# Optimization experiments

Measured on AMD Instinct MI355X. Metric: run time of the kernel, lower is better.

## Reference

```python
import jax, jax.numpy as jnp
import numpy as np
from jax import lax

DIM = 192
HEADS = 4
HIDDEN = int(DIM * 2.66)  # 510


def _conv1x1(x, w, b):
    # x: [B,C,H,W], w: [O,C], b: [O]
    return jnp.einsum('bchw,oc->bohw', x, w) + b[None, :, None, None]


def _dwconv3x3(x, w, b):
    # x: [B,C,H,W], w: [C,1,3,3], b: [C]
    c = x.shape[1]
    y = lax.conv_general_dilated(x, w, window_strides=(1, 1), padding='SAME',
                                 feature_group_count=c,
                                 dimension_numbers=('NCHW', 'OIHW', 'NCHW'))
    return y + b[None, :, None, None]


def _layernorm_c(x, w, b):
    # LayerNorm over channel dim (torch LayerNorm(dim) applied to b,(hw),c)
    mu = jnp.mean(x, axis=1, keepdims=True)
    var = jnp.mean((x - mu) ** 2, axis=1, keepdims=True)
    xn = (x - mu) / jnp.sqrt(var + 1e-5)
    return xn * w[None, :, None, None] + b[None, :, None, None]


def _l2norm(x):
    # F.normalize(dim=-1), eps=1e-12
    n = jnp.sqrt(jnp.sum(x * x, axis=-1, keepdims=True))
    return x / jnp.maximum(n, 1e-12)


def setup_inputs() -> dict:
    key = jax.random.key(0)
    ks = jax.random.split(key, 16)
    s = 0.02
    d, h2 = DIM, HIDDEN * 2
    return {
        'x': jax.random.normal(ks[0], (4, DIM, 128, 128), jnp.float32),
        'ln1_w': jnp.ones((d,), jnp.float32),
        'ln1_b': jnp.zeros((d,), jnp.float32),
        'qkv_w': jax.random.normal(ks[1], (3 * d, d), jnp.float32) * s,
        'qkv_b': jnp.zeros((3 * d,), jnp.float32),
        'qkv_dw_w': jax.random.normal(ks[2], (3 * d, 1, 3, 3), jnp.float32) * s,
        'qkv_dw_b': jnp.zeros((3 * d,), jnp.float32),
        'temperature': jnp.ones((HEADS, 1, 1), jnp.float32),
        'proj_w': jax.random.normal(ks[3], (d, d), jnp.float32) * s,
        'proj_b': jnp.zeros((d,), jnp.float32),
        'ln2_w': jnp.ones((d,), jnp.float32),
        'ln2_b': jnp.zeros((d,), jnp.float32),
        'pin_w': jax.random.normal(ks[4], (h2, d), jnp.float32) * s,
        'pin_b': jnp.zeros((h2,), jnp.float32),
        'dw_w': jax.random.normal(ks[5], (h2, 1, 3, 3), jnp.float32) * s,
        'dw_b': jnp.zeros((h2,), jnp.float32),
        'pout_w': jax.random.normal(ks[6], (d, HIDDEN), jnp.float32) * s,
        'pout_b': jnp.zeros((d,), jnp.float32),
    }


def _attention(x, qkv_w, qkv_b, qkv_dw_w, qkv_dw_b, temperature, proj_w, proj_b):
    b, c, h, w = x.shape
    qkv = _dwconv3x3(_conv1x1(x, qkv_w, qkv_b), qkv_dw_w, qkv_dw_b)
    q, k, v = jnp.split(qkv, 3, axis=1)
    ch = c // HEADS

    def heads(t):  # b (head c) h w -> b head c (h w)
        return t.reshape(b, HEADS, ch, h * w)

    q, k, v = heads(q), heads(k), heads(v)
    q = _l2norm(q)
    k = _l2norm(k)
    attn = jnp.einsum('bhcn,bhdn->bhcd', q, k) * temperature[None]  # [b,H,ch,ch]
    attn = jax.nn.softmax(attn, axis=-1)
    out = jnp.einsum('bhcd,bhdn->bhcn', attn, v)
    out = out.reshape(b, c, h, w)
    return _conv1x1(out, proj_w, proj_b)


def _ffn(x, pin_w, pin_b, dw_w, dw_b, pout_w, pout_b):
    y = _conv1x1(x, pin_w, pin_b)
    y = _dwconv3x3(y, dw_w, dw_b)
    x1, x2 = jnp.split(y, 2, axis=1)
    y = jax.nn.gelu(x1, approximate=False) * x2
    return _conv1x1(y, pout_w, pout_b)


def reference(x, ln1_w, ln1_b, qkv_w, qkv_b, qkv_dw_w, qkv_dw_b, temperature,
              proj_w, proj_b, ln2_w, ln2_b, pin_w, pin_b, dw_w, dw_b,
              pout_w, pout_b):
    x = x + _attention(_layernorm_c(x, ln1_w, ln1_b), qkv_w, qkv_b,
                       qkv_dw_w, qkv_dw_b, temperature, proj_w, proj_b)
    x = x + _ffn(_layernorm_c(x, ln2_w, ln2_b), pin_w, pin_b, dw_w, dw_b,
                 pout_w, pout_b)
    return x
```

## Files before the change

### kernel.cpp

```cpp
#include <hip/hip_runtime.h>
#include <math.h>

typedef long long i64;
typedef unsigned short u16;
typedef unsigned int u32;

#define HW 16384
#define DIM 192
#define NHEADS 4
#define CH 48
#define OQKV 576
#define HID 510
#define H2 1020
#define NB 4
#define NSPLIT 64
#define QKSTR 264

typedef __attribute__((ext_vector_type(8))) short short8v;
typedef __attribute__((ext_vector_type(4))) float float4v;

__device__ __forceinline__ u32 pk(float a, float b) {
  u32 r;
  asm("v_cvt_pk_bf16_f32 %0, %1, %2" : "=v"(r) : "v"(a), "v"(b));
  return r;
}
__device__ __forceinline__ u16 f2bf(float f) {
  union { float f; u32 u; } v; v.f = f;
  u32 r = v.u + 0x7FFF + ((v.u >> 16) & 1);
  return (u16)(r >> 16);
}
__device__ __forceinline__ float bflo(u32 w) {
  union { u32 u; float f; } v; v.u = w << 16; return v.f;
}
__device__ __forceinline__ float bfhi(u32 w) {
  union { u32 u; float f; } v; v.u = w & 0xFFFF0000u; return v.f;
}
__device__ __forceinline__ float bf1(u16 h) {
  union { u32 u; float f; } v; v.u = ((u32)h) << 16; return v.f;
}
__device__ __forceinline__ float gelu_s(float x) {
  return x / (1.f + __expf(-1.702f * x));
}

#define GLL16(gp, lp) __builtin_amdgcn_global_load_lds( \
    (const __attribute__((address_space(1))) u32*)(gp), \
    (__attribute__((address_space(3))) u32*)(lp), 16, 0, 0)

__global__ __launch_bounds__(256) void ln_kernel(const float* __restrict__ x,
    const float* __restrict__ w, const float* __restrict__ b, u16* __restrict__ yT) {
  __shared__ float st[32][193];
  __shared__ float red[2][8][32];
  __shared__ float murs[2][32];
  const float* xb = x + (i64)blockIdx.y * DIM * HW;
  u16* yb = yT + (i64)blockIdx.y * (i64)HW * DIM;
  int tid = threadIdx.x;
  int g = tid >> 5, p = tid & 31;
  int pix0 = blockIdx.x * 32;
  float s = 0.f, ss = 0.f;
  #pragma unroll
  for (int i = 0; i < 24; ++i) {
    float t = xb[(i64)(g * 24 + i) * HW + pix0 + p];
    st[p][g * 24 + i] = t; s += t; ss += t * t;
  }
  red[0][g][p] = s; red[1][g][p] = ss;
  __syncthreads();
  if (tid < 32) {
    float S = 0.f, SS = 0.f;
    #pragma unroll
    for (int gg = 0; gg < 8; ++gg) { S += red[0][gg][tid]; SS += red[1][gg][tid]; }
    float mu = S * (1.f / DIM);
    float var = SS * (1.f / DIM) - mu * mu;
    murs[0][tid] = mu;
    murs[1][tid] = rsqrtf(var + 1e-5f);
  }
  __syncthreads();
  int px = tid >> 3, c0 = (tid & 7) * 24;
  float mu = murs[0][px], rs = murs[1][px];
  u32 ob[12];
  #pragma unroll
  for (int i = 0; i < 24; i += 2) {
    float va = (st[px][c0 + i + 0] - mu) * rs * w[c0 + i + 0] + b[c0 + i + 0];
    float vb = (st[px][c0 + i + 1] - mu) * rs * w[c0 + i + 1] + b[c0 + i + 1];
    ob[i >> 1] = pk(va, vb);
  }
  u16* yp = yb + (i64)(pix0 + px) * DIM + c0;
  #pragma unroll
  for (int j = 0; j < 3; ++j) *(uint4*)(yp + j * 8) = *(const uint4*)&ob[j * 4];
}

__global__ __launch_bounds__(256) void wconv_all(const float* __restrict__ qkv_w,
    const float* __restrict__ proj_w, const float* __restrict__ pin_w,
    const float* __restrict__ pout_w, u16* __restrict__ Wq, u16* __restrict__ Wpj,
    u16* __restrict__ Wpi, u16* __restrict__ Wpo) {
  int idx = blockIdx.x * 256 + threadIdx.x;
  const float* src; u16* dst; int O, C, Kpad;
  if (idx < 122880)      { src = qkv_w;  dst = Wq;  O = OQKV; C = 192; Kpad = 192; }
  else if (idx < 172032) { idx -= 122880; src = proj_w; dst = Wpj; O = 192;  C = 192; Kpad = 192; }
  else if (idx < 368640) { idx -= 172032; src = pin_w;  dst = Wpi; O = H2;   C = 192; Kpad = 192; }
  else if (idx < 499712) { idx -= 368640; src = pout_w; dst = Wpo; O = 192;  C = HID; Kpad = 512; }
  else return;
  int r = idx / Kpad, c = idx - r * Kpad;
  dst[idx] = f2bf((r < O && c < C) ? src[(i64)r * C + c] : 0.f);
}

__global__ __launch_bounds__(256) void gemm_bf16(const u16* __restrict__ A,
    const float* __restrict__ bias, const u16* __restrict__ B,
    const float* __restrict__ Res, float* __restrict__ Out,
    u16* __restrict__ OutB, int O, int K, i64 sB, i64 sOut, i64 sRes) {
  __shared__ __align__(16) u16 lds[2 * 128 * 64];
  int zb = blockIdx.z;
  B += (i64)zb * sB;
  if (Res) Res += (i64)zb * sRes;
  if (OutB) OutB += (i64)zb * sOut; else Out += (i64)zb * sOut;
  int tid = threadIdx.x;
  int lane = tid & 63, wave = tid >> 6;
  int wm = (wave >> 1) * 64, wn = (wave & 1) * 64;
  int obase = blockIdx.y * 128, nbase = blockIdx.x * 128;
  float4v acc[4][4];
  #pragma unroll
  for (int m = 0; m < 4; ++m)
    #pragma unroll
    for (int n = 0; n < 4; ++n) acc[m][n] = (float4v){0.f, 0.f, 0.f, 0.f};

  const u16* Abase = A + (i64)obase * K;
  const u16* Bbase = B + (i64)nbase * K;
  char* ldsA = (char*)&lds[0];
  char* ldsB = (char*)&lds[8192];
  int srow = wave * 8 + (lane >> 3);
  int sj = lane & 7;

  for (int k0 = 0; k0 < K; k0 += 64) {
    #pragma unroll
    for (int iss = 0; iss < 4; ++iss) {
      int r = iss * 32 + srow;
      int kb = sj ^ (r & 7);
      GLL16(Abase + (i64)r * K + k0 + kb * 8, ldsA + iss * 4096 + wave * 1024);
      GLL16(Bbase + (i64)r * K + k0 + kb * 8, ldsB + iss * 4096 + wave * 1024);
    }
    __syncthreads();
    #pragma unroll
    for (int kk = 0; kk < 2; ++kk) {
      short8v af[4], bfr[4];
      #pragma unroll
      for (int m = 0; m < 4; ++m) {
        int r = wm + m * 16 + (lane & 15);
        int kb = kk * 4 + (lane >> 4);
        af[m] = *(const short8v*)(ldsA + r * 128 + ((kb ^ (r & 7)) << 4));
      }
      #pragma unroll
      for (int n = 0; n < 4; ++n) {
        int r = wn + n * 16 + (lane & 15);
        int kb = kk * 4 + (lane >> 4);
        bfr[n] = *(const short8v*)(ldsB + r * 128 + ((kb ^ (r & 7)) << 4));
      }
      #pragma unroll
      for (int m = 0; m < 4; ++m)
        #pragma unroll
        for (int n = 0; n < 4; ++n)
          acc[m][n] = __builtin_amdgcn_mfma_f32_16x16x32_bf16(af[m], bfr[n], acc[m][n], 0, 0, 0);
    }
    __syncthreads();
  }

  int rowq = lane >> 4, coln = lane & 15;
  if (OutB) {
    #pragma unroll
    for (int m = 0; m < 4; ++m) {
      #pragma unroll
      for (int reg = 0; reg < 4; ++reg) {
        int o = wm + m * 16 + rowq * 4 + reg;
        int oo = obase + o;
        float bv = (oo < O) ? bias[oo] : 0.f;
        #pragma unroll
        for (int n = 0; n < 4; n += 2) {
          u32 w2 = pk(acc[m][n][reg] + bv, acc[m][n + 1][reg] + bv);
          lds[o * 128 + wn + n * 16 + coln] = (u16)w2;
          lds[o * 128 + wn + (n + 1) * 16 + coln] = (u16)(w2 >> 16);
        }
      }
    }
    __syncthreads();
    const u32* st32 = (const u32*)lds;
    #pragma unroll
    for (int k = 0; k < 32; ++k) {
      int idx = k * 256 + tid;
      int o = idx >> 6, cd = idx & 63;
      if (obase + o < O)
        ((u32*)(OutB + (i64)(obase + o) * HW + nbase))[cd] = st32[o * 64 + cd];
    }
  } else {
    #pragma unroll
    for (int m = 0; m < 4; ++m) {
      #pragma unroll
      for (int reg = 0; reg < 4; ++reg) {
        int o = obase + wm + m * 16 + rowq * 4 + reg;
        if (o >= O) continue;
        float bv = bias[o];
        #pragma unroll
        for (int n = 0; n < 4; ++n) {
          int nn = nbase + wn + n * 16 + coln;
          float v = acc[m][n][reg] + bv;
          if (Res) v += Res[(i64)o * HW + nn];
          Out[(i64)o * HW + nn] = v;
        }
      }
    }
  }
}

__global__ __launch_bounds__(64) void gemm_skinny(const u16* __restrict__ A,
    const float* __restrict__ bias, const u16* __restrict__ B,
    const float* __restrict__ Res, float* __restrict__ Out,
    int K, i64 sB, i64 sOut, i64 sRes) {
  int zb = blockIdx.y;
  B   += (i64)zb * sB;
  Res += (i64)zb * sRes;
  Out += (i64)zb * sOut;
  int lane = threadIdx.x;
  int r = lane & 15, kq = lane >> 4;
  int nbase = blockIdx.x * 32;
  float4v acc[12][2];
  #pragma unroll
  for (int mi = 0; mi < 12; ++mi) {
    acc[mi][0] = (float4v){0.f, 0.f, 0.f, 0.f};
    acc[mi][1] = (float4v){0.f, 0.f, 0.f, 0.f};
  }
  const u16* Ap = A + (i64)r * K + kq * 8;
  const u16* Bp0 = B + (i64)(nbase + r) * K + kq * 8;
  const u16* Bp1 = Bp0 + (i64)16 * K;
  for (int ks = 0; ks < K; ks += 32) {
    short8v b0 = *(const short8v*)(Bp0 + ks);
    short8v b1 = *(const short8v*)(Bp1 + ks);
    #pragma unroll
    for (int mi = 0; mi < 12; ++mi) {
      short8v a = *(const short8v*)(Ap + (i64)mi * 16 * K + ks);
      acc[mi][0] = __builtin_amdgcn_mfma_f32_16x16x32_bf16(a, b0, acc[mi][0], 0, 0, 0);
      acc[mi][1] = __builtin_amdgcn_mfma_f32_16x16x32_bf16(a, b1, acc[mi][1], 0, 0, 0);
    }
  }
  #pragma unroll
  for (int mi = 0; mi < 12; ++mi) {
    #pragma unroll
    for (int reg = 0; reg < 4; ++reg) {
      int o = mi * 16 + kq * 4 + reg;
      float bv = bias[o];
      #pragma unroll
      for (int ni = 0; ni < 2; ++ni) {
        int n = nbase + ni * 16 + r;
        Out[(i64)o * HW + n] = acc[mi][ni][reg] + bv + Res[(i64)o * HW + n];
      }
    }
  }
}

__global__ __launch_bounds__(256) void dwconv_bf16(const u16* __restrict__ in,
    const float* __restrict__ w9, const float* __restrict__ bs,
    u16* __restrict__ out) {
  in  += (i64)blockIdx.z * OQKV * HW;
  out += (i64)blockIdx.z * OQKV * HW;
  int q = threadIdx.x & 31;
  int grp = threadIdx.x >> 5;
  int y0 = blockIdx.y * 2;
  int c0 = blockIdx.x * 64 + grp * 8;
  int xb = q * 4;
  #pragma unroll
  for (int i = 0; i < 8; ++i) {
    int c = c0 + i;
    const float* wp = w9 + c * 9;
    float bv = bs[c];
    const u16* chan = in + (i64)c * HW;
    float f[4][6];
    #pragma unroll
    for (int r4 = 0; r4 < 4; ++r4) {
      int yy = y0 - 1 + r4;
      if (yy < 0 || yy >= 128) {
        #pragma unroll
        for (int e = 0; e < 6; ++e) f[r4][e] = 0.f;
      } else {
        uint4 raw = *(const uint4*)(chan + yy * 128 + xb - 2);
        f[r4][0] = (q == 0) ? 0.f : bfhi(raw.x);
        f[r4][1] = bflo(raw.y); f[r4][2] = bfhi(raw.y);
        f[r4][3] = bflo(raw.z); f[r4][4] = bfhi(raw.z);
        f[r4][5] = (q == 31) ? 0.f : bflo(raw.w);
      }
    }
    #pragma unroll
    for (int rr = 0; rr < 2; ++rr) {
      float a0 = bv, a1 = bv, a2 = bv, a3 = bv;
      #pragma unroll
      for (int dy = 0; dy < 3; ++dy) {
        float wa = wp[dy * 3 + 0], wb = wp[dy * 3 + 1], wc = wp[dy * 3 + 2];
        const float* fr = f[rr + dy];
        a0 += wa * fr[0] + wb * fr[1] + wc * fr[2];
        a1 += wa * fr[1] + wb * fr[2] + wc * fr[3];
        a2 += wa * fr[2] + wb * fr[3] + wc * fr[4];
        a3 += wa * fr[3] + wb * fr[4] + wc * fr[5];
      }
      uint2 o2;
      o2.x = pk(a0, a1);
      o2.y = pk(a2, a3);
      *(uint2*)(out + (i64)c * HW + (y0 + rr) * 128 + xb) = o2;
    }
  }
}

__global__ __launch_bounds__(256) void l2inv_bf16(const u16* __restrict__ qkv,
    float* __restrict__ inv) {
  int ch = blockIdx.x;
  const u16* p = qkv + (i64)blockIdx.y * OQKV * HW + (i64)ch * HW;
  float s = 0.f;
  for (int i = threadIdx.x * 8; i < HW; i += 256 * 8) {
    uint4 raw = *(const uint4*)(p + i);
    float v0 = bflo(raw.x), v1 = bfhi(raw.x);
    float v2 = bflo(raw.y), v3 = bfhi(raw.y);
    float v4 = bflo(raw.z), v5 = bfhi(raw.z);
    float v6 = bflo(raw.w), v7 = bfhi(raw.w);
    s += v0 * v0 + v1 * v1 + v2 * v2 + v3 * v3 + v4 * v4 + v5 * v5 + v6 * v6 + v7 * v7;
  }
  #pragma unroll
  for (int m = 32; m; m >>= 1) s += __shfl_xor(s, m);
  __shared__ float wsum[4];
  int lane = threadIdx.x & 63, wid = threadIdx.x >> 6;
  if (lane == 0) wsum[wid] = s;
  __syncthreads();
  if (threadIdx.x == 0) {
    float t = wsum[0] + wsum[1] + wsum[2] + wsum[3];
    inv[(i64)blockIdx.y * 384 + ch] = 1.f / fmaxf(sqrtf(t), 1e-12f);
  }
}

__global__ __launch_bounds__(256) void attn_qk_mfma(const u16* __restrict__ qkv,
    float* __restrict__ part) {
  qkv  += (i64)blockIdx.z * OQKV * HW;
  part += (i64)blockIdx.z * 589824;
  __shared__ __align__(16) u16 qs[48][QKSTR];
  __shared__ __align__(16) u16 ks[48][QKSTR];
  int h = blockIdx.x, spb = blockIdx.y;
  int n0 = spb * 1024;
  const u16* qb = qkv + (i64)(h * CH) * HW;
  const u16* kb = qkv + (i64)(DIM + h * CH) * HW;
  int tid = threadIdx.x;
  int lane = tid & 63, wave = tid >> 6;
  float4v acc[3][3];
  #pragma unroll
  for (int i = 0; i < 3; ++i)
    #pragma unroll
    for (int j = 0; j < 3; ++j) acc[i][j] = (float4v){0.f, 0.f, 0.f, 0.f};

  for (int it = 0; it < 4; ++it) {
    int base = n0 + it * 256;
    for (int l = tid; l < 1536; l += 256) {
      int r = l >> 5, j = (l & 31) * 8;
      *(uint4*)&qs[r][j] = *(const uint4*)(qb + (i64)r * HW + base + j);
      *(uint4*)&ks[r][j] = *(const uint4*)(kb + (i64)r * HW + base + j);
    }
    __syncthreads();
    int kbase = wave * 64;
    #pragma unroll
    for (int ksi = 0; ksi < 2; ++ksi) {
      int kofs = kbase + ksi * 32 + (lane >> 4) * 8;
      short8v aq[3], bk[3];
      #pragma unroll
      for (int t = 0; t < 3; ++t) {
        aq[t] = *(const short8v*)&qs[t * 16 + (lane & 15)][kofs];
        bk[t] = *(const short8v*)&ks[t * 16 + (lane & 15)][kofs];
      }
      #pragma unroll
      for (int ci = 0; ci < 3; ++ci)
        #pragma unroll
        for (int di = 0; di < 3; ++di)
          acc[ci][di] = __builtin_amdgcn_mfma_f32_16x16x32_bf16(aq[ci], bk[di], acc[ci][di], 0, 0, 0);
    }
    __syncthreads();
  }
  int rowq = lane >> 4, coln = lane & 15;
  float* pp = part + ((i64)(h * NSPLIT) + spb * 4 + wave) * 2304;
  #pragma unroll
  for (int ci = 0; ci < 3; ++ci)
    #pragma unroll
    for (int reg = 0; reg < 4; ++reg) {
      int c = ci * 16 + rowq * 4 + reg;
      #pragma unroll
      for (int di = 0; di < 3; ++di)
        pp[c * 48 + di * 16 + coln] = acc[ci][di][reg];
    }
}

__global__ __launch_bounds__(64) void attn_sm3(const float* __restrict__ part,
    const float* __restrict__ inv, const float* __restrict__ temp,
    float* __restrict__ attn) {
  part += (i64)blockIdx.z * 589824;
  attn += (i64)blockIdx.z * 9216;
  const float* invb = inv + (i64)blockIdx.z * 384;
  int h = blockIdx.x, c = blockIdx.y;
  int d = threadIdx.x;
  float logit = -1e30f;
  if (d < CH) {
    float s = 0.f;
    for (int sp = 0; sp < NSPLIT; ++sp)
      s += part[((i64)(h * NSPLIT) + sp) * 2304 + c * 48 + d];
    logit = s * invb[h * CH + c] * invb[192 + h * CH + d] * temp[h];
  }
  float m = logit;
  #pragma unroll
  for (int mask = 32; mask; mask >>= 1) m = fmaxf(m, __shfl_xor(m, mask));
  float e = (d < CH) ? expf(logit - m) : 0.f;
  float ssum = e;
  #pragma unroll
  for (int mask = 32; mask; mask >>= 1) ssum += __shfl_xor(ssum, mask);
  if (d < CH) attn[(i64)h * 2304 + c * 48 + d] = e / ssum;
}

__global__ __launch_bounds__(256) void attn_v_kernel(const u16* __restrict__ qkv,
    const float* __restrict__ attnm, u16* __restrict__ outT) {
  qkv   += (i64)blockIdx.z * OQKV * HW;
  attnm += (i64)blockIdx.z * 9216;
  outT  += (i64)blockIdx.z * (i64)HW * DIM;
  __shared__ float as[CH * CH];
  __shared__ u16 st[256 * 52];
  int h = blockIdx.x, tile = blockIdx.y;
  int tid = threadIdx.x;
  for (int l = tid; l < CH * CH; l += 256) as[l] = attnm[(i64)h * 2304 + l];
  __syncthreads();
  int n = tile * 256 + tid;
  const u16* vb = qkv + (i64)(2 * DIM + h * CH) * HW + n;
  float vreg[CH];
  #pragma unroll
  for (int d = 0; d < CH; ++d) vreg[d] = bf1(vb[(i64)d * HW]);
  u32* strow = (u32*)st + tid * 26;
  #pragma unroll 2
  for (int c = 0; c < CH; c += 4) {
    float a0 = 0.f, a1 = 0.f, a2 = 0.f, a3 = 0.f;
    const float* r0 = &as[(c + 0) * CH];
    const float* r1 = &as[(c + 1) * CH];
    const float* r2 = &as[(c + 2) * CH];
    const float* r3 = &as[(c + 3) * CH];
    #pragma unroll
    for (int d = 0; d < CH; ++d) {
      float vv = vreg[d];
      a0 += r0[d] * vv; a1 += r1[d] * vv; a2 += r2[d] * vv; a3 += r3[d] * vv;
    }
    strow[(c >> 1) + 0] = pk(a0, a1);
    strow[(c >> 1) + 1] = pk(a2, a3);
  }
  __syncthreads();
  const uint2* sv = (const uint2*)st;
  u16* ob = outT + (i64)(tile * 256) * DIM + h * CH;
  #pragma unroll
  for (int k = 0; k < 12; ++k) {
    int idx = k * 256 + tid;
    int px = idx / 12, pc = idx - px * 12;
    *(uint2*)(ob + (i64)px * DIM + pc * 4) = sv[px * 13 + pc];
  }
}

__global__ __launch_bounds__(256) void dwgate_bf16(const u16* __restrict__ h1,
    const float* __restrict__ w9, const float* __restrict__ bs,
    u16* __restrict__ og) {
  h1 += (i64)blockIdx.z * H2 * HW;
  og += (i64)blockIdx.z * (i64)HW * 512;
  __shared__ u32 st[128 * 17];
  int q = threadIdx.x & 31;
  int grp = threadIdx.x >> 5;
  int y = blockIdx.y;
  int c0 = blockIdx.x * 32 + grp * 4;
  int xb = q * 4;
  float prev[4];
  #pragma unroll
  for (int i = 0; i < 4; ++i) {
    int c = c0 + i;
    bool valid = (c < HID);
    float b1 = valid ? bs[c] : 0.f;
    float b2 = valid ? bs[c + HID] : 0.f;
    float a0 = b1, a1 = b1, a2 = b1, a3 = b1;
    float g0 = b2, g1 = b2, g2 = b2, g3 = b2;
    if (valid) {
      const float* wp1 = w9 + c * 9;
      const float* wp2 = w9 + (i64)(c + HID) * 9;
      const u16* ch1 = h1 + (i64)c * HW;
      const u16* ch2 = h1 + (i64)(c + HID) * HW;
      #pragma unroll
      for (int dy = -1; dy <= 1; ++dy) {
        int yy = y + dy;
        if (yy < 0 || yy >= 128) continue;
        {
          uint4 raw = *(const uint4*)(ch1 + yy * 128 + xb - 2);
          float f1 = bfhi(raw.x);
          float f2 = bflo(raw.y), f3 = bfhi(raw.y);
          float f4 = bflo(raw.z), f5 = bfhi(raw.z);
          float f6 = bflo(raw.w);
          if (q == 0) f1 = 0.f;
          if (q == 31) f6 = 0.f;
          float wa = wp1[(dy + 1) * 3 + 0], wb = wp1[(dy + 1) * 3 + 1], wc = wp1[(dy + 1) * 3 + 2];
          a0 += wa * f1 + wb * f2 + wc * f3;
          a1 += wa * f2 + wb * f3 + wc * f4;
          a2 += wa * f3 + wb * f4 + wc * f5;
          a3 += wa * f4 + wb * f5 + wc * f6;
        }
        {
          uint4 raw = *(const uint4*)(ch2 + yy * 128 + xb - 2);
          float f1 = bfhi(raw.x);
          float f2 = bflo(raw.y), f3 = bfhi(raw.y);
          float f4 = bflo(raw.z), f5 = bfhi(raw.z);
          float f6 = bflo(raw.w);
          if (q == 0) f1 = 0.f;
          if (q == 31) f6 = 0.f;
          float wa = wp2[(dy + 1) * 3 + 0], wb = wp2[(dy + 1) * 3 + 1], wc = wp2[(dy + 1) * 3 + 2];
          g0 += wa * f1 + wb * f2 + wc * f3;
          g1 += wa * f2 + wb * f3 + wc * f4;
          g2 += wa * f3 + wb * f4 + wc * f5;
          g3 += wa * f4 + wb * f5 + wc * f6;
        }
      }
    }
    float r0 = valid ? gelu_s(a0) * g0 : 0.f;
    float r1 = valid ? gelu_s(a1) * g1 : 0.f;
    float r2 = valid ? gelu_s(a2) * g2 : 0.f;
    float r3 = valid ? gelu_s(a3) * g3 : 0.f;
    if (i & 1) {
      int dwi = grp * 2 + (i >> 1);
      st[(xb + 0) * 17 + dwi] = pk(prev[0], r0);
      st[(xb + 1) * 17 + dwi] = pk(prev[1], r1);
      st[(xb + 2) * 17 + dwi] = pk(prev[2], r2);
      st[(xb + 3) * 17 + dwi] = pk(prev[3], r3);
    } else {
      prev[0] = r0; prev[1] = r1; prev[2] = r2; prev[3] = r3;
    }
  }
  __syncthreads();
  u32* og32 = (u32*)og;
  int tid = threadIdx.x;
  #pragma unroll
  for (int k = 0; k < 8; ++k) {
    int idx = k * 256 + tid;
    int px = idx >> 4, dwi = idx & 15;
    og32[(i64)(y * 128 + px) * 256 + blockIdx.x * 16 + dwi] = st[px * 17 + dwi];
  }
}

extern "C" void kernel_launch(void* const* d_in, const int* in_sizes, int n_in,
                              void* d_out, int out_size, void* d_ws, size_t ws_size,
                              hipStream_t stream) {
  const float* x        = (const float*)d_in[0];
  const float* ln1_w    = (const float*)d_in[1];
  const float* ln1_b    = (const float*)d_in[2];
  const float* qkv_w    = (const float*)d_in[3];
  const float* qkv_b    = (const float*)d_in[4];
  const float* qkv_dw_w = (const float*)d_in[5];
  const float* qkv_dw_b = (const float*)d_in[6];
  const float* temp     = (const float*)d_in[7];
  const float* proj_w   = (const float*)d_in[8];
  const float* proj_b   = (const float*)d_in[9];
  const float* ln2_w    = (const float*)d_in[10];
  const float* ln2_b    = (const float*)d_in[11];
  const float* pin_w    = (const float*)d_in[12];
  const float* pin_b    = (const float*)d_in[13];
  const float* dw_w     = (const float*)d_in[14];
  const float* dw_b     = (const float*)d_in[15];
  const float* pout_w   = (const float*)d_in[16];
  const float* pout_b   = (const float*)d_in[17];
  float* out = (float*)d_out;
  char* ws = (char*)d_ws;

  u16* Wq   = (u16*)ws;
  u16* Wpj  = Wq + 640 * 192;
  u16* Wpi  = Wpj + 256 * 192;
  u16* Wpo  = Wpi + 1024 * 192;
  u16* yT   = Wpo + 256 * 512;
  char* dyn = (char*)(yT + (i64)NB * HW * DIM);

  auto layout = [&](int nb, float*& attnm, float*& part, float*& invv,
                    u16*& bufA, u16*& bufQ) -> size_t {
    char* p = dyn;
    attnm = (float*)p; p += (i64)nb * 9216 * 4;
    part  = (float*)p; p += (i64)nb * 589824 * 4;
    invv  = (float*)p; p += (i64)nb * 384 * 4;
    bufA  = (u16*)p;   p += (i64)nb * H2 * HW * 2;
    bufQ  = (u16*)p;   p += (i64)nb * OQKV * HW * 2;
    return (size_t)(p - ws);
  };

  float *attnm, *part, *invv; u16 *bufA, *bufQ;
  int nbat = 4;
  if (layout(4, attnm, part, invv, bufA, bufQ) > ws_size) {
    nbat = 1;
    if (layout(1, attnm, part, invv, bufA, bufQ) > ws_size) return;
  }

  wconv_all<<<(499712 + 255) / 256, 256, 0, stream>>>(qkv_w, proj_w, pin_w, pout_w,
                                                      Wq, Wpj, Wpi, Wpo);
  ln_kernel<<<dim3(HW / 32, NB), 256, 0, stream>>>(x, ln1_w, ln1_b, yT);

  for (int b0 = 0; b0 < NB; b0 += nbat) {
    const float* xb = x + (i64)b0 * DIM * HW;
    float* outb = out + (i64)b0 * DIM * HW;
    u16* yTb = yT + (i64)b0 * HW * DIM;
    u16* attnoutT = bufA;
    u16* gatedT = bufQ;

    gemm_bf16<<<dim3(HW / 128, 5, nbat), 256, 0, stream>>>(
        Wq, qkv_b, yTb, nullptr, nullptr, bufA, OQKV, DIM,
        (i64)HW * DIM, (i64)OQKV * HW, 0);
    dwconv_bf16<<<dim3(OQKV / 64, 64, nbat), 256, 0, stream>>>(bufA, qkv_dw_w, qkv_dw_b, bufQ);
    l2inv_bf16<<<dim3(384, nbat), 256, 0, stream>>>(bufQ, invv);
    attn_qk_mfma<<<dim3(NHEADS, 16, nbat), 256, 0, stream>>>(bufQ, part);
    attn_sm3<<<dim3(NHEADS, CH, nbat), 64, 0, stream>>>(part, invv, temp, attnm);
    attn_v_kernel<<<dim3(NHEADS, HW / 256, nbat), 256, 0, stream>>>(bufQ, attnm, attnoutT);
    gemm_skinny<<<dim3(HW / 32, nbat), 64, 0, stream>>>(
        Wpj, proj_b, attnoutT, xb, outb, DIM,
        (i64)HW * DIM, (i64)DIM * HW, (i64)DIM * HW);

    ln_kernel<<<dim3(HW / 32, nbat), 256, 0, stream>>>(outb, ln2_w, ln2_b, yTb);
    gemm_bf16<<<dim3(HW / 128, 8, nbat), 256, 0, stream>>>(
        Wpi, pin_b, yTb, nullptr, nullptr, bufA, H2, DIM,
        (i64)HW * DIM, (i64)H2 * HW, 0);
    dwgate_bf16<<<dim3(16, 128, nbat), 256, 0, stream>>>(bufA, dw_w, dw_b, gatedT);
    gemm_skinny<<<dim3(HW / 32, nbat), 64, 0, stream>>>(
        Wpo, pout_b, gatedT, outb, outb, 512,
        (i64)HW * 512, (i64)DIM * HW, (i64)DIM * HW);
  }
}
```

Before: 436.1 us.

## Fuse LayerNorm2 into projection GEMM epilogue and register-block dwgate rows

The attention output-projection GEMM now computes the residual sum, then in its epilogue computes per-pixel channel mean and variance with cross-lane shuffles and writes the LayerNorm2 output in bf16. This removes the separate ln_kernel launch and its re-read of the fp32 output. Separately, the FFN depthwise-conv+gate kernel now computes two output rows per block, reusing 4 loaded input rows instead of 3 loads per row, which halves the grid. The costs are higher register pressure and a one-pass variance formula (E[x^2]-mu^2) that is less numerically robust.

```diff
diff --git a/kernel.cpp b/kernel.cpp
--- a/kernel.cpp
+++ b/kernel.cpp
@@ -253,6 +253,82 @@
   }
 }
 
+__global__ __launch_bounds__(64) void gemm_skinny_ln(const u16* __restrict__ A,
+    const float* __restrict__ bias, const u16* __restrict__ B,
+    const float* __restrict__ Res, float* __restrict__ Out,
+    u16* __restrict__ yT, const float* __restrict__ lnw, const float* __restrict__ lnb,
+    int K, i64 sB, i64 sOut, i64 sRes) {
+  int zb = blockIdx.y;
+  B   += (i64)zb * sB;
+  Res += (i64)zb * sRes;
+  Out += (i64)zb * sOut;
+  yT  += (i64)zb * (i64)HW * DIM;
+  int lane = threadIdx.x;
+  int r = lane & 15, kq = lane >> 4;
+  int nbase = blockIdx.x * 32;
+  float4v acc[12][2];
+  #pragma unroll
+  for (int mi = 0; mi < 12; ++mi) {
+    acc[mi][0] = (float4v){0.f, 0.f, 0.f, 0.f};
+    acc[mi][1] = (float4v){0.f, 0.f, 0.f, 0.f};
+  }
+  const u16* Ap = A + (i64)r * K + kq * 8;
+  const u16* Bp0 = B + (i64)(nbase + r) * K + kq * 8;
+  const u16* Bp1 = Bp0 + (i64)16 * K;
+  for (int ks = 0; ks < K; ks += 32) {
+    short8v b0 = *(const short8v*)(Bp0 + ks);
+    short8v b1 = *(const short8v*)(Bp1 + ks);
+    #pragma unroll
+    for (int mi = 0; mi < 12; ++mi) {
+      short8v a = *(const short8v*)(Ap + (i64)mi * 16 * K + ks);
+      acc[mi][0] = __builtin_amdgcn_mfma_f32_16x16x32_bf16(a, b0, acc[mi][0], 0, 0, 0);
+      acc[mi][1] = __builtin_amdgcn_mfma_f32_16x16x32_bf16(a, b1, acc[mi][1], 0, 0, 0);
+    }
+  }
+  float s[2] = {0.f, 0.f}, ss[2] = {0.f, 0.f};
+  #pragma unroll
+  for (int mi = 0; mi < 12; ++mi) {
+    #pragma unroll
+    for (int reg = 0; reg < 4; ++reg) {
+      int o = mi * 16 + kq * 4 + reg;
+      float bv = bias[o];
+      #pragma unroll
+      for (int ni = 0; ni < 2; ++ni) {
+        int n = nbase + ni * 16 + r;
+        float v = acc[mi][ni][reg] + bv + Res[(i64)o * HW + n];
+        Out[(i64)o * HW + n] = v;
+        acc[mi][ni][reg] = v;
+        s[ni] += v; ss[ni] += v * v;
+      }
+    }
+  }
+  float mu[2], rsg[2];
+  #pragma unroll
+  for (int ni = 0; ni < 2; ++ni) {
+    float S = s[ni], SS = ss[ni];
+    S += __shfl_xor(S, 16); S += __shfl_xor(S, 32);
+    SS += __shfl_xor(SS, 16); SS += __shfl_xor(SS, 32);
+    float m = S * (1.f / DIM);
+    mu[ni] = m;
+    rsg[ni] = rsqrtf(SS * (1.f / DIM) - m * m + 1e-5f);
+  }
+  #pragma unroll
+  for (int mi = 0; mi < 12; ++mi) {
+    int o0 = mi * 16 + kq * 4;
+    float w0 = lnw[o0], w1 = lnw[o0 + 1], w2 = lnw[o0 + 2], w3 = lnw[o0 + 3];
+    float c0 = lnb[o0], c1 = lnb[o0 + 1], c2 = lnb[o0 + 2], c3 = lnb[o0 + 3];
+    #pragma unroll
+    for (int ni = 0; ni < 2; ++ni) {
+      int n = nbase + ni * 16 + r;
+      float m = mu[ni], rg = rsg[ni];
+      uint2 u;
+      u.x = pk((acc[mi][ni][0] - m) * rg * w0 + c0, (acc[mi][ni][1] - m) * rg * w1 + c1);
+      u.y = pk((acc[mi][ni][2] - m) * rg * w2 + c2, (acc[mi][ni][3] - m) * rg * w3 + c3);
+      *(uint2*)(yT + (i64)n * DIM + o0) = u;
+    }
+  }
+}
+
 __global__ __launch_bounds__(256) void dwconv_bf16(const u16* __restrict__ in,
     const float* __restrict__ w9, const float* __restrict__ bs,
     u16* __restrict__ out) {
@@ -459,82 +535,118 @@
     u16* __restrict__ og) {
   h1 += (i64)blockIdx.z * H2 * HW;
   og += (i64)blockIdx.z * (i64)HW * 512;
-  __shared__ u32 st[128 * 17];
+  __shared__ u32 st[2][128 * 17];
   int q = threadIdx.x & 31;
   int grp = threadIdx.x >> 5;
-  int y = blockIdx.y;
+  int y0 = blockIdx.y * 2;
   int c0 = blockIdx.x * 32 + grp * 4;
   int xb = q * 4;
-  float prev[4];
+  float prev[2][4];
   #pragma unroll
   for (int i = 0; i < 4; ++i) {
     int c = c0 + i;
     bool valid = (c < HID);
-    float b1 = valid ? bs[c] : 0.f;
-    float b2 = valid ? bs[c + HID] : 0.f;
-    float a0 = b1, a1 = b1, a2 = b1, a3 = b1;
-    float g0 = b2, g1 = b2, g2 = b2, g3 = b2;
+    float a[2][4], g[2][4];
+    float f[4][6];
     if (valid) {
-      const float* wp1 = w9 + c * 9;
-      const float* wp2 = w9 + (i64)(c + HID) * 9;
-      const u16* ch1 = h1 + (i64)c * HW;
-      const u16* ch2 = h1 + (i64)(c + HID) * HW;
-      #pragma unroll
-      for (int dy = -1; dy <= 1; ++dy) {
-        int yy = y + dy;
-        if (yy < 0 || yy >= 128) continue;
-        {
-          uint4 raw = *(const uint4*)(ch1 + yy * 128 + xb - 2);
-          float f1 = bfhi(raw.x);
-          float f2 = bflo(raw.y), f3 = bfhi(raw.y);
-          float f4 = bflo(raw.z), f5 = bfhi(raw.z);
-          float f6 = bflo(raw.w);
-          if (q == 0) f1 = 0.f;
-          if (q == 31) f6 = 0.f;
-          float wa = wp1[(dy + 1) * 3 + 0], wb = wp1[(dy + 1) * 3 + 1], wc = wp1[(dy + 1) * 3 + 2];
-          a0 += wa * f1 + wb * f2 + wc * f3;
-          a1 += wa * f2 + wb * f3 + wc * f4;
-          a2 += wa * f3 + wb * f4 + wc * f5;
-          a3 += wa * f4 + wb * f5 + wc * f6;
+      {
+        const float* wp = w9 + c * 9;
+        float bv = bs[c];
+        const u16* chan = h1 + (i64)c * HW;
+        #pragma unroll
+        for (int r4 = 0; r4 < 4; ++r4) {
+          int yy = y0 - 1 + r4;
+          if (yy < 0 || yy >= 128) {
+            #pragma unroll
+            for (int e = 0; e < 6; ++e) f[r4][e] = 0.f;
+          } else {
+            uint4 raw = *(const uint4*)(chan + yy * 128 + xb - 2);
+            f[r4][0] = (q == 0) ? 0.f : bfhi(raw.x);
+            f[r4][1] = bflo(raw.y); f[r4][2] = bfhi(raw.y);
+            f[r4][3] = bflo(raw.z); f[r4][4] = bfhi(raw.z);
+            f[r4][5] = (q == 31) ? 0.f : bflo(raw.w);
+          }
         }
-        {
-          uint4 raw = *(const uint4*)(ch2 + yy * 128 + xb - 2);
-          float f1 = bfhi(raw.x);
-          float f2 = bflo(raw.y), f3 = bfhi(raw.y);
-          float f4 = bflo(raw.z), f5 = bfhi(raw.z);
-          float f6 = bflo(raw.w);
-          if (q == 0) f1 = 0.f;
-          if (q == 31) f6 = 0.f;
-          float wa = wp2[(dy + 1) * 3 + 0], wb = wp2[(dy + 1) * 3 + 1], wc = wp2[(dy + 1) * 3 + 2];
-          g0 += wa * f1 + wb * f2 + wc * f3;
-          g1 += wa * f2 + wb * f3 + wc * f4;
-          g2 += wa * f3 + wb * f4 + wc * f5;
-          g3 += wa * f4 + wb * f5 + wc * f6;
+        #pragma unroll
+        for (int rr = 0; rr < 2; ++rr) {
+          float a0 = bv, a1 = bv, a2 = bv, a3 = bv;
+          #pragma unroll
+          for (int dy = 0; dy < 3; ++dy) {
+            float wa = wp[dy * 3 + 0], wb = wp[dy * 3 + 1], wc = wp[dy * 3 + 2];
+            const float* fr = f[rr + dy];
+            a0 += wa * fr[0] + wb * fr[1] + wc * fr[2];
+            a1 += wa * fr[1] + wb * fr[2] + wc * fr[3];
+            a2 += wa * fr[2] + wb * fr[3] + wc * fr[4];
+            a3 += wa * fr[3] + wb * fr[4] + wc * fr[5];
+          }
+          a[rr][0] = a0; a[rr][1] = a1; a[rr][2] = a2; a[rr][3] = a3;
         }
       }
-    }
-    float r0 = valid ? gelu_s(a0) * g0 : 0.f;
-    float r1 = valid ? gelu_s(a1) * g1 : 0.f;
-    float r2 = valid ? gelu_s(a2) * g2 : 0.f;
-    float r3 = valid ? gelu_s(a3) * g3 : 0.f;
+      {
+        const float* wp = w9 + (i64)(c + HID) * 9;
+        float bv = bs[c + HID];
+        const u16* chan = h1 + (i64)(c + HID) * HW;
+        #pragma unroll
+        for (int r4 = 0; r4 < 4; ++r4) {
+          int yy = y0 - 1 + r4;
+          if (yy < 0 || yy >= 128) {
+            #pragma unroll
+            for (int e = 0; e < 6; ++e) f[r4][e] = 0.f;
+          } else {
+            uint4 raw = *(const uint4*)(chan + yy * 128 + xb - 2);
+            f[r4][0] = (q == 0) ? 0.f : bfhi(raw.x);
+            f[r4][1] = bflo(raw.y); f[r4][2] = bfhi(raw.y);
+            f[r4][3] = bflo(raw.z); f[r4][4] = bfhi(raw.z);
+            f[r4][5] = (q == 31) ? 0.f : bflo(raw.w);
+          }
+        }
+        #pragma unroll
+        for (int rr = 0; rr < 2; ++rr) {
+          float g0 = bv, g1 = bv, g2 = bv, g3 = bv;
+          #pragma unroll
+          for (int dy = 0; dy < 3; ++dy) {
+            float wa = wp[dy * 3 + 0], wb = wp[dy * 3 + 1], wc = wp[dy * 3 + 2];
+            const float* fr = f[rr + dy];
+            g0 += wa * fr[0] + wb * fr[1] + wc * fr[2];
+            g1 += wa * fr[1] + wb * fr[2] + wc * fr[3];
+            g2 += wa * fr[2] + wb * fr[3] + wc * fr[4];
+            g3 += wa * fr[3] + wb * fr[4] + wc * fr[5];
+          }
+          g[rr][0] = g0; g[rr][1] = g1; g[rr][2] = g2; g[rr][3] = g3;
+        }
+      }
+    }
+    float res[2][4];
+    #pragma unroll
+    for (int rr = 0; rr < 2; ++rr)
+      #pragma unroll
+      for (int j = 0; j < 4; ++j)
+        res[rr][j] = valid ? gelu_s(a[rr][j]) * g[rr][j] : 0.f;
     if (i & 1) {
       int dwi = grp * 2 + (i >> 1);
-      st[(xb + 0) * 17 + dwi] = pk(prev[0], r0);
-      st[(xb + 1) * 17 + dwi] = pk(prev[1], r1);
-      st[(xb + 2) * 17 + dwi] = pk(prev[2], r2);
-      st[(xb + 3) * 17 + dwi] = pk(prev[3], r3);
+      #pragma unroll
+      for (int rr = 0; rr < 2; ++rr)
+        #pragma unroll
+        for (int j = 0; j < 4; ++j)
+          st[rr][(xb + j) * 17 + dwi] = pk(prev[rr][j], res[rr][j]);
     } else {
-      prev[0] = r0; prev[1] = r1; prev[2] = r2; prev[3] = r3;
+      #pragma unroll
+      for (int rr = 0; rr < 2; ++rr)
+        #pragma unroll
+        for (int j = 0; j < 4; ++j) prev[rr][j] = res[rr][j];
     }
   }
   __syncthreads();
   u32* og32 = (u32*)og;
   int tid = threadIdx.x;
   #pragma unroll
-  for (int k = 0; k < 8; ++k) {
-    int idx = k * 256 + tid;
-    int px = idx >> 4, dwi = idx & 15;
-    og32[(i64)(y * 128 + px) * 256 + blockIdx.x * 16 + dwi] = st[px * 17 + dwi];
+  for (int rr = 0; rr < 2; ++rr) {
+    #pragma unroll
+    for (int k = 0; k < 8; ++k) {
+      int idx = k * 256 + tid;
+      int px = idx >> 4, dwi = idx & 15;
+      og32[(i64)((y0 + rr) * 128 + px) * 256 + blockIdx.x * 16 + dwi] = st[rr][px * 17 + dwi];
+    }
   }
 }
 
@@ -606,15 +718,14 @@
     attn_qk_mfma<<<dim3(NHEADS, 16, nbat), 256, 0, stream>>>(bufQ, part);
     attn_sm3<<<dim3(NHEADS, CH, nbat), 64, 0, stream>>>(part, invv, temp, attnm);
     attn_v_kernel<<<dim3(NHEADS, HW / 256, nbat), 256, 0, stream>>>(bufQ, attnm, attnoutT);
-    gemm_skinny<<<dim3(HW / 32, nbat), 64, 0, stream>>>(
-        Wpj, proj_b, attnoutT, xb, outb, DIM,
+    gemm_skinny_ln<<<dim3(HW / 32, nbat), 64, 0, stream>>>(
+        Wpj, proj_b, attnoutT, xb, outb, yTb, ln2_w, ln2_b, DIM,
         (i64)HW * DIM, (i64)DIM * HW, (i64)DIM * HW);
 
-    ln_kernel<<<dim3(HW / 32, nbat), 256, 0, stream>>>(outb, ln2_w, ln2_b, yTb);
     gemm_bf16<<<dim3(HW / 128, 8, nbat), 256, 0, stream>>>(
         Wpi, pin_b, yTb, nullptr, nullptr, bufA, H2, DIM,
         (i64)HW * DIM, (i64)H2 * HW, 0);
-    dwgate_bf16<<<dim3(16, 128, nbat), 256, 0, stream>>>(bufA, dw_w, dw_b, gatedT);
+    dwgate_bf16<<<dim3(16, 64, nbat), 256, 0, stream>>>(bufA, dw_w, dw_b, gatedT);
     gemm_skinny<<<dim3(HW / 32, nbat), 64, 0, stream>>>(
         Wpo, pout_b, gatedT, outb, outb, 512,
         (i64)HW * 512, (i64)DIM * HW, (i64)DIM * HW);
```

After: 440.0 us. No clear change (+0.9%).
